# Performance work log

Measured on AMD Instinct MI355X. Metric: run time of the kernel, lower is better.

## Reference

```python
import jax, jax.numpy as jnp
import numpy as np

EPS = 1e-06

def setup_inputs() -> dict:
    key = jax.random.key(0)
    k1, k2, k3, k4 = jax.random.split(key, 4)
    N, E, D = 100000, 1600000, 128
    feat = jax.random.normal(k1, (N, D), dtype=jnp.float32)
    src = jax.random.randint(k2, (E,), 0, N, dtype=jnp.int32)
    dst = jax.random.randint(k3, (E,), 0, N, dtype=jnp.int32)
    W = jax.random.normal(k4, (D, D), dtype=jnp.float32) * 0.05
    b = jnp.zeros((D,), dtype=jnp.float32)
    a2 = jnp.ones((D,), dtype=jnp.float32)
    b2 = jnp.zeros((D,), dtype=jnp.float32)
    return {"feat": feat, "src": src, "dst": dst, "W": W, "b": b, "a2": a2, "b2": b2}

def reference(feat, src, dst, W, b, a2, b2):
    N, D = feat.shape
    # LayerNorm (torch std is unbiased, eps added to std, not var)
    mean = jnp.mean(feat, axis=-1, keepdims=True)
    std = jnp.std(feat, axis=-1, keepdims=True, ddof=1)
    h = a2 * (feat - mean) / (std + EPS) + b2
    # DGL GraphConv, norm='both': D_out^{-1/2} gather-sum D_in^{-1/2}, then W, b, relu
    ones = jnp.ones(src.shape[0], dtype=feat.dtype)
    out_deg = jax.ops.segment_sum(ones, src, num_segments=N)
    in_deg = jax.ops.segment_sum(ones, dst, num_segments=N)
    norm_out = jax.lax.rsqrt(jnp.maximum(out_deg, 1.0))[:, None]
    norm_in = jax.lax.rsqrt(jnp.maximum(in_deg, 1.0))[:, None]
    h = h * norm_out
    # in_feats == out_feats -> DGL multiplies weight first
    h = h @ W
    agg = jax.ops.segment_sum(h[src], dst, num_segments=N)  # [N, D]
    rst = agg * norm_in + b
    rst = jax.nn.relu(rst)
    # residual (Identity since in_feats == out_feats); dropout is identity at eval
    return rst + feat
```

## Files before the change

### kernel.cpp

```cpp
#include <hip/hip_runtime.h>

#define D 128
#define BSH 6
#define BN 64
#define NBUK_MAX 2048
#define NBLK 256
#define SRT_CAP 2048
#define NW_LDS 25600

__device__ __forceinline__ unsigned short f2bf(float f) {
    unsigned u = __float_as_uint(f);
    unsigned r = (u + 0x7FFF + ((u >> 16) & 1)) >> 16;
    return (unsigned short)r;
}
__device__ __forceinline__ float bf2f(unsigned short s) {
    return __uint_as_float(((unsigned)s) << 16);
}

__global__ __launch_bounds__(1024) void count_kernel(const int* __restrict__ src,
        const int* __restrict__ dst, int* __restrict__ hist,
        unsigned* __restrict__ partial, int E, int nbuk, int chunk, int NW) {
    __shared__ unsigned ph[NW_LDS];
    __shared__ int hb[NBUK_MAX];
    int t = threadIdx.x;
    for (int i = t; i < NW_LDS; i += 1024) ph[i] = 0;
    for (int i = t; i < nbuk; i += 1024) hb[i] = 0;
    __syncthreads();
    int lo = blockIdx.x * chunk;
    int hi = min(E, lo + chunk);
    for (int e = lo + t; e < hi; e += 1024) {
        int s = src[e], d = dst[e];
        atomicAdd(&ph[s >> 2], 1u << ((s & 3) * 8));
        atomicAdd(&hb[d >> BSH], 1);
    }
    __syncthreads();
    int* hrow = hist + (size_t)blockIdx.x * nbuk;
    for (int i = t; i < nbuk; i += 1024) hrow[i] = hb[i];
    unsigned* prow = partial + (size_t)blockIdx.x * NW;
    for (int i = t; i < NW; i += 1024) prow[i] = ph[i];
}

__global__ __launch_bounds__(1024) void reduce_kernel(const unsigned* __restrict__ partial,
        unsigned* __restrict__ podeg, int NW) {
    __shared__ unsigned acc[16][64];
    int t = threadIdx.x;
    int wl = t & 63, bg = t >> 6;
    int w = blockIdx.x * 64 + wl;
    unsigned s = 0;
    if (w < NW) {
        for (int b = bg; b < NBLK; b += 16) s += partial[(size_t)b * NW + w];
    }
    acc[bg][wl] = s;
    __syncthreads();
    if (bg == 0 && w < NW) {
        unsigned tot = 0;
        #pragma unroll
        for (int g = 0; g < 16; ++g) tot += acc[g][wl];
        podeg[w] = tot;
    }
}

__global__ __launch_bounds__(64) void hscan_kernel(int* __restrict__ hist,
        int* __restrict__ colsum, int nbuk) {
    int buk = blockIdx.x;
    int l = threadIdx.x;
    int v[4]; int s = 0;
    #pragma unroll
    for (int i = 0; i < 4; ++i) {
        v[i] = hist[(size_t)(l * 4 + i) * nbuk + buk];
        s += v[i];
    }
    int x = s;
    #pragma unroll
    for (int m = 1; m < 64; m <<= 1) {
        int y = __shfl_up(x, m);
        if (l >= m) x += y;
    }
    int base = x - s;
    #pragma unroll
    for (int i = 0; i < 4; ++i) {
        int tmp = v[i];
        hist[(size_t)(l * 4 + i) * nbuk + buk] = base;
        base += tmp;
    }
    if (l == 63) colsum[buk] = x;
}

__global__ __launch_bounds__(1024) void bscan_kernel(const int* __restrict__ colsum,
        int* __restrict__ base, int nbuk, int E) {
    __shared__ int s[1024];
    int t = threadIdx.x;
    int i0 = 2 * t, i1 = 2 * t + 1;
    int a = (i0 < nbuk) ? colsum[i0] : 0;
    int c = (i1 < nbuk) ? colsum[i1] : 0;
    int p = a + c;
    s[t] = p;
    __syncthreads();
    #pragma unroll
    for (int off = 1; off < 1024; off <<= 1) {
        int x = (t >= off) ? s[t - off] : 0;
        __syncthreads();
        s[t] += x;
        __syncthreads();
    }
    int ex = s[t] - p;
    if (i0 < nbuk) base[i0] = ex;
    if (i1 < nbuk) base[i1] = ex + a;
    if (t == 0) base[nbuk] = E;
}

__global__ __launch_bounds__(1024) void scatter_kernel(const int* __restrict__ src,
        const int* __restrict__ dst, const int* __restrict__ hist,
        const int* __restrict__ base, unsigned* __restrict__ pairs,
        int E, int nbuk, int chunk) {
    __shared__ int cur[NBUK_MAX];
    int t = threadIdx.x;
    const int* hrow = hist + (size_t)blockIdx.x * nbuk;
    for (int i = t; i < nbuk; i += 1024) cur[i] = base[i] + hrow[i];
    __syncthreads();
    int lo = blockIdx.x * chunk;
    int hi = min(E, lo + chunk);
    for (int e = lo + t; e < hi; e += 1024) {
        int d = dst[e];
        int pos = atomicAdd(&cur[d >> BSH], 1);
        pairs[pos] = ((unsigned)(d & (BN - 1)) << 24) | (unsigned)src[e];
    }
}

__global__ __launch_bounds__(256) void ln_gemm_kernel(const float* __restrict__ feat,
        const float* __restrict__ W, const float* __restrict__ a2, const float* __restrict__ b2,
        const unsigned* __restrict__ podeg, unsigned short* __restrict__ hw, int N) {
    __shared__ float Ws[D * D];
    __shared__ float hs[D][32];

    const int t = threadIdx.x;

    #pragma unroll
    for (int i = 0; i < 16; ++i) {
        int idx = (i * 256 + t) * 4;
        *(float4*)&Ws[idx] = *(const float4*)&W[idx];
    }

    const int r = t >> 3;
    const int sub = t & 7;
    const int grow = blockIdx.x * 32 + r;
    const bool valid = grow < N;

    float4 v[4];
    float sum = 0.f, sumsq = 0.f;
    if (valid) {
        const float4* fr = (const float4*)(feat + (size_t)grow * D + sub * 16);
        #pragma unroll
        for (int i = 0; i < 4; ++i) {
            v[i] = fr[i];
            sum   += v[i].x + v[i].y + v[i].z + v[i].w;
            sumsq += v[i].x * v[i].x + v[i].y * v[i].y + v[i].z * v[i].z + v[i].w * v[i].w;
        }
    }
    #pragma unroll
    for (int m = 1; m < 8; m <<= 1) {
        sum   += __shfl_xor(sum, m);
        sumsq += __shfl_xor(sumsq, m);
    }

    if (valid) {
        float mean = sum * (1.f / 128.f);
        float var  = fmaxf((sumsq - 128.f * mean * mean) * (1.f / 127.f), 0.f);
        float inv  = 1.f / (sqrtf(var) + 1e-6f);
        int   od   = (podeg[grow >> 2] >> ((grow & 3) * 8)) & 0xFF;
        float norm = rsqrtf(fmaxf((float)od, 1.f));
        float sa   = inv * norm;
        #pragma unroll
        for (int i = 0; i < 4; ++i) {
            int k = sub * 16 + i * 4;
            hs[k + 0][r] = a2[k + 0] * (v[i].x - mean) * sa + b2[k + 0] * norm;
            hs[k + 1][r] = a2[k + 1] * (v[i].y - mean) * sa + b2[k + 1] * norm;
            hs[k + 2][r] = a2[k + 2] * (v[i].z - mean) * sa + b2[k + 2] * norm;
            hs[k + 3][r] = a2[k + 3] * (v[i].w - mean) * sa + b2[k + 3] * norm;
        }
    } else {
        #pragma unroll
        for (int i = 0; i < 16; ++i) hs[sub * 16 + i][r] = 0.f;
    }

    __syncthreads();

    const int tx = t & 31;
    const int ty = t >> 5;
    float acc[4][4];
    #pragma unroll
    for (int i = 0; i < 4; ++i)
        #pragma unroll
        for (int j = 0; j < 4; ++j) acc[i][j] = 0.f;

    #pragma unroll 4
    for (int k = 0; k < D; ++k) {
        float4 hv = *(const float4*)&hs[k][ty * 4];
        float4 wv = *(const float4*)&Ws[k * D + tx * 4];
        float ha[4] = {hv.x, hv.y, hv.z, hv.w};
        float wa[4] = {wv.x, wv.y, wv.z, wv.w};
        #pragma unroll
        for (int i = 0; i < 4; ++i)
            #pragma unroll
            for (int j = 0; j < 4; ++j)
                acc[i][j] = fmaf(ha[i], wa[j], acc[i][j]);
    }

    #pragma unroll
    for (int i = 0; i < 4; ++i) {
        int gr = blockIdx.x * 32 + ty * 4 + i;
        if (gr < N) {
            ushort4 o;
            o.x = f2bf(acc[i][0]);
            o.y = f2bf(acc[i][1]);
            o.z = f2bf(acc[i][2]);
            o.w = f2bf(acc[i][3]);
            *(ushort4*)&hw[(size_t)gr * D + tx * 4] = o;
        }
    }
}

__global__ __launch_bounds__(512) void gather_kernel(const unsigned* __restrict__ pairs,
        const int* __restrict__ bukbase, const unsigned short* __restrict__ hw,
        const float* __restrict__ feat, const float* __restrict__ bias,
        float* __restrict__ out, int N) {
    __shared__ unsigned srt[SRT_CAP];
    __shared__ int cnt[BN];
    __shared__ int ofs[BN + 1];

    int t = threadIdx.x;
    int buk = blockIdx.x;
    int beg = bukbase[buk];
    int ne = bukbase[buk + 1] - beg;
    if (ne > SRT_CAP) ne = SRT_CAP;

    if (t < BN) cnt[t] = 0;
    __syncthreads();

    for (int i = t; i < ne; i += 512)
        atomicAdd(&cnt[pairs[beg + i] >> 24], 1);
    __syncthreads();

    if (t < BN) {
        int c = cnt[t];
        int x = c;
        #pragma unroll
        for (int m = 1; m < BN; m <<= 1) {
            int y = __shfl_up(x, m);
            if (t >= m) x += y;
        }
        ofs[t] = x - c;
        if (t == BN - 1) ofs[BN] = x;
        cnt[t] = x - c;
    }
    __syncthreads();

    for (int i = t; i < ne; i += 512) {
        unsigned p = pairs[beg + i];
        int pos = atomicAdd(&cnt[p >> 24], 1);
        srt[pos] = p & 0xFFFFFFu;
    }
    __syncthreads();

    int wv = t >> 6;
    int lane = t & 63;
    int co = lane * 2;

    for (int nl = wv; nl < BN; nl += 8) {
        int n = (buk << BSH) + nl;
        if (n >= N) break;
        int s0 = ofs[nl], s1 = ofs[nl + 1];
        int deg = s1 - s0;

        float a0 = 0.f, a1 = 0.f;
        int e = s0;
        for (; e + 3 < s1; e += 4) {
            int x0 = srt[e], x1 = srt[e + 1], x2 = srt[e + 2], x3 = srt[e + 3];
            ushort2 q0 = *(const ushort2*)&hw[(size_t)x0 * D + co];
            ushort2 q1 = *(const ushort2*)&hw[(size_t)x1 * D + co];
            ushort2 q2 = *(const ushort2*)&hw[(size_t)x2 * D + co];
            ushort2 q3 = *(const ushort2*)&hw[(size_t)x3 * D + co];
            a0 += bf2f(q0.x) + bf2f(q1.x) + bf2f(q2.x) + bf2f(q3.x);
            a1 += bf2f(q0.y) + bf2f(q1.y) + bf2f(q2.y) + bf2f(q3.y);
        }
        for (; e < s1; ++e) {
            int x0 = srt[e];
            ushort2 q0 = *(const ushort2*)&hw[(size_t)x0 * D + co];
            a0 += bf2f(q0.x);
            a1 += bf2f(q0.y);
        }

        float ni = rsqrtf(fmaxf((float)deg, 1.f));
        float2 bb = *(const float2*)&bias[co];
        float2 f  = *(const float2*)&feat[(size_t)n * D + co];
        float2 o;
        o.x = fmaxf(fmaf(a0, ni, bb.x), 0.f) + f.x;
        o.y = fmaxf(fmaf(a1, ni, bb.y), 0.f) + f.y;
        *(float2*)&out[(size_t)n * D + co] = o;
    }
}

extern "C" void kernel_launch(void* const* d_in, const int* in_sizes, int n_in,
                              void* d_out, int out_size, void* d_ws, size_t ws_size,
                              hipStream_t stream) {
    const float* feat = (const float*)d_in[0];
    const int*   src  = (const int*)d_in[1];
    const int*   dst  = (const int*)d_in[2];
    const float* W    = (const float*)d_in[3];
    const float* b    = (const float*)d_in[4];
    const float* a2   = (const float*)d_in[5];
    const float* b2   = (const float*)d_in[6];

    const int N = in_sizes[0] / D;
    const int E = in_sizes[1];
    const int NW = (N + 3) / 4;
    const int nbuk = (N + BN - 1) >> BSH;
    const int chunk = (E + NBLK - 1) / NBLK;

    float* out = (float*)d_out;

    unsigned short* hw = (unsigned short*)d_ws;
    unsigned* podeg = (unsigned*)(hw + (size_t)N * D);
    int* hist    = (int*)(podeg + NW);
    int* colsum  = hist + (size_t)NBLK * NBUK_MAX;
    int* bukbase = colsum + NBUK_MAX;
    unsigned* pairs = (unsigned*)(bukbase + (NBUK_MAX + 1));
    unsigned* partial = pairs + E;

    count_kernel<<<NBLK, 1024, 0, stream>>>(src, dst, hist, partial, E, nbuk, chunk, NW);
    reduce_kernel<<<(NW + 63) / 64, 1024, 0, stream>>>(partial, podeg, NW);
    hscan_kernel<<<nbuk, 64, 0, stream>>>(hist, colsum, nbuk);
    bscan_kernel<<<1, 1024, 0, stream>>>(colsum, bukbase, nbuk, E);
    scatter_kernel<<<NBLK, 1024, 0, stream>>>(src, dst, hist, bukbase, pairs, E, nbuk, chunk);

    ln_gemm_kernel<<<(N + 31) / 32, 256, 0, stream>>>(feat, W, a2, b2, podeg, hw, N);

    gather_kernel<<<nbuk, 512, 0, stream>>>(pairs, bukbase, hw, feat, b, out, N);
}
```

Baseline: 181.6 us.

## Use bf16 MFMA with swizzled LDS tiles in LayerNorm+GEMM kernel

Replaces the scalar fp32 FMA GEMM in the LayerNorm+projection kernel with bf16 MFMA 16x16x32 instructions. W is converted to bf16, transposed and XOR-swizzled in LDS, and the normalized activations are also stored as swizzled bf16, with 64 rows per block instead of 32. This aims to cut the compute-bound GEMM cost and the LDS footprint. The trade-off is that both GEMM inputs are rounded to bf16 before the multiply, and the output writes become scalar 2-byte stores per lane.

```diff
diff --git a/kernel.cpp b/kernel.cpp
--- a/kernel.cpp
+++ b/kernel.cpp
@@ -7,6 +7,9 @@
 #define NBLK 256
 #define SRT_CAP 2048
 #define NW_LDS 25600
+
+typedef __bf16 bf16x8 __attribute__((ext_vector_type(8)));
+typedef float  f32x4  __attribute__((ext_vector_type(4)));
 
 __device__ __forceinline__ unsigned short f2bf(float f) {
     unsigned u = __float_as_uint(f);
@@ -130,92 +133,113 @@
 __global__ __launch_bounds__(256) void ln_gemm_kernel(const float* __restrict__ feat,
         const float* __restrict__ W, const float* __restrict__ a2, const float* __restrict__ b2,
         const unsigned* __restrict__ podeg, unsigned short* __restrict__ hw, int N) {
-    __shared__ float Ws[D * D];
-    __shared__ float hs[D][32];
+    __shared__ unsigned short Wt[D * D];
+    __shared__ unsigned short hs[64 * D];
 
     const int t = threadIdx.x;
-
-    #pragma unroll
-    for (int i = 0; i < 16; ++i) {
-        int idx = (i * 256 + t) * 4;
-        *(float4*)&Ws[idx] = *(const float4*)&W[idx];
-    }
-
-    const int r = t >> 3;
-    const int sub = t & 7;
-    const int grow = blockIdx.x * 32 + r;
-    const bool valid = grow < N;
-
-    float4 v[4];
-    float sum = 0.f, sumsq = 0.f;
-    if (valid) {
-        const float4* fr = (const float4*)(feat + (size_t)grow * D + sub * 16);
-        #pragma unroll
-        for (int i = 0; i < 4; ++i) {
-            v[i] = fr[i];
-            sum   += v[i].x + v[i].y + v[i].z + v[i].w;
-            sumsq += v[i].x * v[i].x + v[i].y * v[i].y + v[i].z * v[i].z + v[i].w * v[i].w;
-        }
-    }
-    #pragma unroll
-    for (int m = 1; m < 8; m <<= 1) {
-        sum   += __shfl_xor(sum, m);
-        sumsq += __shfl_xor(sumsq, m);
-    }
-
-    if (valid) {
-        float mean = sum * (1.f / 128.f);
-        float var  = fmaxf((sumsq - 128.f * mean * mean) * (1.f / 127.f), 0.f);
-        float inv  = 1.f / (sqrtf(var) + 1e-6f);
-        int   od   = (podeg[grow >> 2] >> ((grow & 3) * 8)) & 0xFF;
-        float norm = rsqrtf(fmaxf((float)od, 1.f));
-        float sa   = inv * norm;
-        #pragma unroll
-        for (int i = 0; i < 4; ++i) {
-            int k = sub * 16 + i * 4;
-            hs[k + 0][r] = a2[k + 0] * (v[i].x - mean) * sa + b2[k + 0] * norm;
-            hs[k + 1][r] = a2[k + 1] * (v[i].y - mean) * sa + b2[k + 1] * norm;
-            hs[k + 2][r] = a2[k + 2] * (v[i].z - mean) * sa + b2[k + 2] * norm;
-            hs[k + 3][r] = a2[k + 3] * (v[i].w - mean) * sa + b2[k + 3] * norm;
-        }
-    } else {
-        #pragma unroll
-        for (int i = 0; i < 16; ++i) hs[sub * 16 + i][r] = 0.f;
-    }
-
-    __syncthreads();
-
-    const int tx = t & 31;
-    const int ty = t >> 5;
-    float acc[4][4];
-    #pragma unroll
-    for (int i = 0; i < 4; ++i)
-        #pragma unroll
-        for (int j = 0; j < 4; ++j) acc[i][j] = 0.f;
-
-    #pragma unroll 4
-    for (int k = 0; k < D; ++k) {
-        float4 hv = *(const float4*)&hs[k][ty * 4];
-        float4 wv = *(const float4*)&Ws[k * D + tx * 4];
-        float ha[4] = {hv.x, hv.y, hv.z, hv.w};
-        float wa[4] = {wv.x, wv.y, wv.z, wv.w};
-        #pragma unroll
-        for (int i = 0; i < 4; ++i)
-            #pragma unroll
-            for (int j = 0; j < 4; ++j)
-                acc[i][j] = fmaf(ha[i], wa[j], acc[i][j]);
-    }
-
-    #pragma unroll
-    for (int i = 0; i < 4; ++i) {
-        int gr = blockIdx.x * 32 + ty * 4 + i;
-        if (gr < N) {
-            ushort4 o;
-            o.x = f2bf(acc[i][0]);
-            o.y = f2bf(acc[i][1]);
-            o.z = f2bf(acc[i][2]);
-            o.w = f2bf(acc[i][3]);
-            *(ushort4*)&hw[(size_t)gr * D + tx * 4] = o;
+    const int base = blockIdx.x * 64;
+
+    {
+        const float4* W4 = (const float4*)W;
+        #pragma unroll
+        for (int i = 0; i < 16; ++i) {
+            int idx = i * 256 + t;
+            int k = idx >> 5;
+            int c0 = (idx & 31) * 4;
+            float4 wv = W4[idx];
+            Wt[(c0 + 0) * D + (k ^ (((c0 + 0) & 7) << 3))] = f2bf(wv.x);
+            Wt[(c0 + 1) * D + (k ^ (((c0 + 1) & 7) << 3))] = f2bf(wv.y);
+            Wt[(c0 + 2) * D + (k ^ (((c0 + 2) & 7) << 3))] = f2bf(wv.z);
+            Wt[(c0 + 3) * D + (k ^ (((c0 + 3) & 7) << 3))] = f2bf(wv.w);
+        }
+    }
+
+    {
+        const int r = t >> 2;
+        const int sub = t & 3;
+        const int grow = base + r;
+        const bool valid = grow < N;
+
+        float4 v[8];
+        float sum = 0.f, sumsq = 0.f;
+        if (valid) {
+            const float4* fr = (const float4*)(feat + (size_t)grow * D + sub * 32);
+            #pragma unroll
+            for (int i = 0; i < 8; ++i) {
+                v[i] = fr[i];
+                sum   += v[i].x + v[i].y + v[i].z + v[i].w;
+                sumsq += v[i].x * v[i].x + v[i].y * v[i].y + v[i].z * v[i].z + v[i].w * v[i].w;
+            }
+        }
+        sum   += __shfl_xor(sum, 1);   sumsq += __shfl_xor(sumsq, 1);
+        sum   += __shfl_xor(sum, 2);   sumsq += __shfl_xor(sumsq, 2);
+
+        if (valid) {
+            float mean = sum * (1.f / 128.f);
+            float var  = fmaxf((sumsq - 128.f * mean * mean) * (1.f / 127.f), 0.f);
+            float inv  = 1.f / (sqrtf(var) + 1e-6f);
+            int   od   = (podeg[grow >> 2] >> ((grow & 3) * 8)) & 0xFF;
+            float norm = rsqrtf(fmaxf((float)od, 1.f));
+            float sa   = inv * norm;
+            #pragma unroll
+            for (int i = 0; i < 8; ++i) {
+                int c0 = sub * 32 + i * 4;
+                float4 av = *(const float4*)&a2[c0];
+                float4 bv = *(const float4*)&b2[c0];
+                ushort4 o;
+                o.x = f2bf(av.x * (v[i].x - mean) * sa + bv.x * norm);
+                o.y = f2bf(av.y * (v[i].y - mean) * sa + bv.y * norm);
+                o.z = f2bf(av.z * (v[i].z - mean) * sa + bv.z * norm);
+                o.w = f2bf(av.w * (v[i].w - mean) * sa + bv.w * norm);
+                *(ushort4*)&hs[r * D + (c0 ^ ((r & 7) << 3))] = o;
+            }
+        } else {
+            ushort4 z = make_ushort4(0, 0, 0, 0);
+            #pragma unroll
+            for (int i = 0; i < 8; ++i) {
+                int c0 = sub * 32 + i * 4;
+                *(ushort4*)&hs[r * D + (c0 ^ ((r & 7) << 3))] = z;
+            }
+        }
+    }
+    __syncthreads();
+
+    {
+        const int w = t >> 6;
+        const int l = t & 63;
+        const int lrow = l & 15;
+        const int kg = l >> 4;
+        const int arow = w * 16 + lrow;
+
+        bf16x8 a[4];
+        #pragma unroll
+        for (int kt = 0; kt < 4; ++kt) {
+            int col = kt * 32 + kg * 8;
+            a[kt] = *reinterpret_cast<const bf16x8*>(&hs[arow * D + (col ^ ((arow & 7) << 3))]);
+        }
+
+        f32x4 acc[8];
+        #pragma unroll
+        for (int ct = 0; ct < 8; ++ct) acc[ct] = (f32x4){0.f, 0.f, 0.f, 0.f};
+
+        #pragma unroll
+        for (int ct = 0; ct < 8; ++ct) {
+            int brow = ct * 16 + lrow;
+            #pragma unroll
+            for (int kt = 0; kt < 4; ++kt) {
+                int col = kt * 32 + kg * 8;
+                bf16x8 bfr = *reinterpret_cast<const bf16x8*>(&Wt[brow * D + (col ^ ((brow & 7) << 3))]);
+                acc[ct] = __builtin_amdgcn_mfma_f32_16x16x32_bf16(a[kt], bfr, acc[ct], 0, 0, 0);
+            }
+        }
+
+        #pragma unroll
+        for (int ct = 0; ct < 8; ++ct) {
+            #pragma unroll
+            for (int p = 0; p < 4; ++p) {
+                int gr = base + w * 16 + kg * 4 + p;
+                if (gr < N) hw[(size_t)gr * D + ct * 16 + lrow] = f2bf(acc[ct][p]);
+            }
         }
     }
 }
@@ -333,7 +357,7 @@
     bscan_kernel<<<1, 1024, 0, stream>>>(colsum, bukbase, nbuk, E);
     scatter_kernel<<<NBLK, 1024, 0, stream>>>(src, dst, hist, bukbase, pairs, E, nbuk, chunk);
 
-    ln_gemm_kernel<<<(N + 31) / 32, 256, 0, stream>>>(feat, W, a2, b2, podeg, hw, N);
+    ln_gemm_kernel<<<(N + 63) / 64, 256, 0, stream>>>(feat, W, a2, b2, podeg, hw, N);
 
     gather_kernel<<<nbuk, 512, 0, stream>>>(pairs, bukbase, hw, feat, b, out, N);
 }
```

New measurement: 158.7 us. 12.7% less time.
